# Optimization experiments

Hardware: AMD Instinct MI355X
Metric: run time of the kernel (lower is better)

## Reference

```python
import jax, jax.numpy as jnp
import numpy as np

B, N, E = 16, 1024, 256
H, D = 16, 16            # head_num * qkv_dim == embedding_dim
FF = 2 * E               # ff_size = embedding_dim * 2
EPS = 1e-5


def setup_inputs() -> dict:
    key = jax.random.key(0)
    ks = jax.random.split(key, 12)
    s = lambda fan_in: 1.0 / np.sqrt(fan_in)
    return {
        "x":  jax.random.normal(ks[0], (B, N, E), dtype=jnp.float32),
        # attention projections (nn.Linear, bias=False) stored as [in, out]
        "Wq": jax.random.uniform(ks[1], (E, H * D), jnp.float32, -s(E), s(E)),
        "Wk": jax.random.uniform(ks[2], (E, H * D), jnp.float32, -s(E), s(E)),
        "Wv": jax.random.uniform(ks[3], (E, H * D), jnp.float32, -s(E), s(E)),
        "Wo": jax.random.uniform(ks[4], (H * D, E), jnp.float32, -s(H * D), s(H * D)),
        "bo": jax.random.uniform(ks[5], (E,), jnp.float32, -s(H * D), s(H * D)),
        # InstanceNorm1d affine params
        "gamma1": jnp.ones((E,), jnp.float32),
        "beta1":  jnp.zeros((E,), jnp.float32),
        "gamma2": jnp.ones((E,), jnp.float32),
        "beta2":  jnp.zeros((E,), jnp.float32),
        # SwiGLU FFN: Linear(E, 2*FF) -> SwiGLU -> Linear(FF, E)
        "W1": jax.random.uniform(ks[6], (E, 2 * FF), jnp.float32, -s(E), s(E)),
        "b1": jax.random.uniform(ks[7], (2 * FF,), jnp.float32, -s(E), s(E)),
        "W2": jax.random.uniform(ks[8], (FF, E), jnp.float32, -s(FF), s(FF)),
        "b2": jax.random.uniform(ks[9], (E,), jnp.float32, -s(FF), s(FF)),
    }


def _instance_norm(x, gamma, beta):
    # x: [B, N, E]; normalize over N per (batch, channel), biased variance
    mean = jnp.mean(x, axis=1, keepdims=True)
    var = jnp.mean(jnp.square(x - mean), axis=1, keepdims=True)
    return (x - mean) * jax.lax.rsqrt(var + EPS) * gamma + beta


def reference(x, Wq, Wk, Wv, Wo, bo, gamma1, beta1, gamma2, beta2, W1, b1, W2, b2):
    b, n, e = x.shape
    q = (x @ Wq).reshape(b, n, H, D)
    k = (x @ Wk).reshape(b, n, H, D)
    v = (x @ Wv).reshape(b, n, H, D)
    scores = jnp.einsum("bnhd,bmhd->bhnm", q, k) / np.sqrt(D)   # [B,H,N,N]
    weights = jax.nn.softmax(scores, axis=-1)
    attn = jnp.einsum("bhnm,bmhd->bnhd", weights, v).reshape(b, n, H * D)
    mha = attn @ Wo + bo
    h = _instance_norm(mha + x, gamma1, beta1)
    # SwiGLU FFN: chunk -> (x_part, gate); silu(gate) * x_part
    proj = h @ W1 + b1
    x_part, gate = proj[..., :FF], proj[..., FF:]
    ff = (jax.nn.silu(gate) * x_part) @ W2 + b2
    return _instance_norm(h + ff, gamma2, beta2)
```

## Files before the change

### kernel.cpp

```cpp
#include <hip/hip_runtime.h>
#include <stdint.h>

typedef unsigned short u16;
typedef __bf16 bf16x8 __attribute__((ext_vector_type(8)));
typedef float f32x4 __attribute__((ext_vector_type(4)));

__device__ __forceinline__ float bf2f(u16 v){ return __uint_as_float(((unsigned)v)<<16); }
__device__ __forceinline__ u16 f2bf(float f){
  unsigned u = __float_as_uint(f);
  unsigned r = (u + 0x7FFFu + ((u>>16)&1u)) >> 16;
  return (u16)r;
}
__device__ __forceinline__ float fexp2(float x){
#if __has_builtin(__builtin_amdgcn_exp2f)
  return __builtin_amdgcn_exp2f(x);
#else
  return exp2f(x);
#endif
}

__global__ void transpose_all(const float* __restrict__ Wq, const float* __restrict__ Wk,
                              const float* __restrict__ Wv, const float* __restrict__ Wo,
                              const float* __restrict__ W1, const float* __restrict__ W2,
                              u16* __restrict__ wqkvT, u16* __restrict__ woT,
                              u16* __restrict__ w1T, u16* __restrict__ w2T)
{
  __shared__ u16 tile[32][33];
  int bid = blockIdx.x;
  const float* in; u16* out; int K, N, t2; bool glu = false;
  if (bid < 64)       { in = Wq; out = wqkvT;           K = 256; N = 256;  t2 = bid; }
  else if (bid < 128) { in = Wk; out = wqkvT + 65536;   K = 256; N = 256;  t2 = bid - 64; }
  else if (bid < 192) { in = Wv; out = wqkvT + 131072;  K = 256; N = 256;  t2 = bid - 128; }
  else if (bid < 256) { in = Wo; out = woT;             K = 256; N = 256;  t2 = bid - 192; }
  else if (bid < 512) { in = W1; out = w1T;             K = 256; N = 1024; t2 = bid - 256; glu = true; }
  else                { in = W2; out = w2T;             K = 512; N = 256;  t2 = bid - 512; }
  int ntn = N >> 5;
  int k0 = (t2 / ntn) * 32, n0 = (t2 % ntn) * 32;
  int t = threadIdx.x;
  #pragma unroll
  for (int p = 0; p < 4; ++p) {
    int u = t + p * 256; int r = u >> 5, c = u & 31;
    tile[r][c] = f2bf(in[(size_t)(k0 + r) * N + n0 + c]);
  }
  __syncthreads();
  #pragma unroll
  for (int p = 0; p < 4; ++p) {
    int u = t + p * 256; int r = u >> 5, c = u & 31;
    int q = n0 + r;
    int row = glu ? (q < 512 ? 2 * q : 2 * (q - 512) + 1) : q;
    out[(size_t)row * K + k0 + c] = tile[c][r];
  }
}

__global__ void xconv(const float* __restrict__ x, u16* __restrict__ xb)
{
  int idx = (blockIdx.x * 256 + threadIdx.x) * 8;
  float4 a0 = *(const float4*)(x + idx);
  float4 a1 = *(const float4*)(x + idx + 4);
  union { u16 u[8]; uint4 v; } pk;
  pk.u[0] = f2bf(a0.x); pk.u[1] = f2bf(a0.y); pk.u[2] = f2bf(a0.z); pk.u[3] = f2bf(a0.w);
  pk.u[4] = f2bf(a1.x); pk.u[5] = f2bf(a1.y); pk.u[6] = f2bf(a1.z); pk.u[7] = f2bf(a1.w);
  *(uint4*)(xb + idx) = pk.v;
}

enum { MODE_QKV = 0, MODE_Y_RES = 1, MODE_GLU = 2 };

template<int MODE, int RESF32, int STATS>
__launch_bounds__(256, 2)
__global__ void gemm_kernel(const u16* __restrict__ A, const u16* __restrict__ BT,
                            int M, int N, int K,
                            const float* __restrict__ bias, const void* __restrict__ resp,
                            u16* __restrict__ outB,
                            float* __restrict__ ssum, float* __restrict__ ssq)
{
  __shared__ u16 As[128 * 40];
  __shared__ u16 Bs[128 * 40];
  const int t = threadIdx.x;
  const int m0 = blockIdx.x * 128;
  const int n0 = blockIdx.y * 128;
  const int lane = t & 63;
  const int w = t >> 6;
  const int wm = (w >> 1) * 64;
  const int wn = (w & 1) * 64;
  const int fr = lane & 15;
  const int fg = lane >> 4;

  f32x4 acc[4][4];
  #pragma unroll
  for (int i = 0; i < 4; ++i)
    #pragma unroll
    for (int j = 0; j < 4; ++j)
      acc[i][j] = (f32x4){0.f, 0.f, 0.f, 0.f};

  for (int k0 = 0; k0 < K; k0 += 32) {
    __syncthreads();
    #pragma unroll
    for (int p = 0; p < 2; ++p) {
      int u = t + p * 256;
      int row = u >> 2, cb = u & 3;
      float4 va = *(const float4*)(A + (size_t)(m0 + row) * K + k0 + cb * 8);
      *(float4*)(As + row * 40 + cb * 8) = va;
      float4 vb = *(const float4*)(BT + (size_t)(n0 + row) * K + k0 + cb * 8);
      *(float4*)(Bs + row * 40 + cb * 8) = vb;
    }
    __syncthreads();
    bf16x8 af[4], bfr[4];
    #pragma unroll
    for (int i = 0; i < 4; ++i) af[i]  = *(const bf16x8*)(As + (wm + i * 16 + fr) * 40 + fg * 8);
    #pragma unroll
    for (int j = 0; j < 4; ++j) bfr[j] = *(const bf16x8*)(Bs + (wn + j * 16 + fr) * 40 + fg * 8);
    #pragma unroll
    for (int i = 0; i < 4; ++i)
      #pragma unroll
      for (int j = 0; j < 4; ++j)
        acc[i][j] = __builtin_amdgcn_mfma_f32_16x16x32_bf16(af[i], bfr[j], acc[i][j], 0, 0, 0);
  }

  const int bIdx = m0 >> 10;
  #pragma unroll
  for (int j = 0; j < 4; ++j) {
    int col = n0 + wn + j * 16 + fr;
    float bv = 0.f;
    if (MODE == MODE_Y_RES) bv = bias[col];
    if (MODE == MODE_GLU)   bv = bias[(col >> 1) + ((col & 1) << 9)];
    float sj = 0.f, qj = 0.f;
    #pragma unroll
    for (int i = 0; i < 4; ++i) {
      #pragma unroll
      for (int r = 0; r < 4; ++r) {
        int row = m0 + wm + i * 16 + fg * 4 + r;
        float v = acc[i][j][r] + bv;
        if (MODE == MODE_QKV) {
          int which = col >> 8, h = (col >> 4) & 15, d = col & 15;
          int b = row >> 10, ns = row & 1023;
          outB[(size_t)which * 4194304 + (((size_t)(b * 16 + h) * 1024 + ns) * 16 + d)] = f2bf(v);
        } else if (MODE == MODE_Y_RES) {
          size_t idx = (size_t)row * N + col;
          float rv = RESF32 ? ((const float*)resp)[idx] : bf2f(((const u16*)resp)[idx]);
          float y = v + rv;
          outB[idx] = f2bf(y);
          if (STATS) { sj += y; qj += y * y; }
        } else {
          float partner = __shfl_xor(v, 1);
          if ((fr & 1) == 0) {
            float g = partner / (1.f + __expf(-partner));
            outB[(size_t)row * 512 + (col >> 1)] = f2bf(g * v);
          }
        }
      }
    }
    if (STATS) {
      sj += __shfl_xor(sj, 16); sj += __shfl_xor(sj, 32);
      qj += __shfl_xor(qj, 16); qj += __shfl_xor(qj, 32);
      if (fg == 0) {
        atomicAdd(&ssum[bIdx * 256 + col], sj);
        atomicAdd(&ssq[bIdx * 256 + col], qj);
      }
    }
  }
}

#define SCALE_L2 0.360673760222241f

__launch_bounds__(512, 4)
__global__ void attn_kernel(const u16* __restrict__ Q, const u16* __restrict__ Kg,
                            const u16* __restrict__ Vg, u16* __restrict__ attn)
{
  __shared__ u16 Ks[64 * 24];
  __shared__ u16 Vt[16 * 72];
  __shared__ u16 Pb[8 * 16 * 72];
  const int t = threadIdx.x;
  const int bh = blockIdx.x >> 3;
  const int qg = blockIdx.x & 7;
  const int b = bh >> 4, h = bh & 15;
  const size_t base = (size_t)bh * 16384;
  const int w = t >> 6, lane = t & 63;
  const int fr = lane & 15, fg = lane >> 4;
  u16* Pw = Pb + w * (16 * 72);
  const int q0 = qg * 128 + w * 16;
  const f32x4 zero4 = (f32x4){0.f, 0.f, 0.f, 0.f};

  bf16x8 qf = {};
  if (fg < 2) {
    union { u16 u[8]; uint4 v; bf16x8 f; } qt;
    qt.v = *(const uint4*)(Q + base + (size_t)(q0 + fr) * 16 + fg * 8);
    #pragma unroll
    for (int j = 0; j < 8; ++j) qt.u[j] = f2bf(bf2f(qt.u[j]) * SCALE_L2);
    qf = qt.f;
  }

  f32x4 acco = zero4;
  float lsum[4] = {0.f, 0.f, 0.f, 0.f};

  for (int kc = 0; kc < 1024; kc += 64) {
    __syncthreads();
    if (t < 128) {
      int row = t >> 1, half = t & 1;
      uint4 v = *(const uint4*)(Kg + base + (size_t)(kc + row) * 16 + half * 8);
      *(uint4*)(Ks + row * 24 + half * 8) = v;
    } else if (t < 256) {
      int u = t - 128;
      int row = u >> 1, half = u & 1;
      const u16* src = Vg + base + (size_t)(kc + row) * 16 + half * 8;
      int idx = row & 31, sub = row >> 5;
      int pos = sub * 32 + (idx < 16 ? 2 * idx : 2 * (idx - 16) + 1);
      #pragma unroll
      for (int j = 0; j < 8; ++j) Vt[(half * 8 + j) * 72 + pos] = src[j];
    }
    __syncthreads();

    #pragma unroll
    for (int sub = 0; sub < 2; ++sub) {
      const int kb = sub * 32;
      bf16x8 kf0 = {}, kf1 = {};
      if (fg < 2) {
        kf0 = *(const bf16x8*)(Ks + (kb + fr) * 24 + fg * 8);
        kf1 = *(const bf16x8*)(Ks + (kb + 16 + fr) * 24 + fg * 8);
      }
      f32x4 s0 = __builtin_amdgcn_mfma_f32_16x16x32_bf16(qf, kf0, zero4, 0, 0, 0);
      f32x4 s1 = __builtin_amdgcn_mfma_f32_16x16x32_bf16(qf, kf1, zero4, 0, 0, 0);
      #pragma unroll
      for (int r = 0; r < 4; ++r) {
        float p0 = fexp2(s0[r]);
        float p1 = fexp2(s1[r]);
        lsum[r] += p0 + p1;
        *(unsigned*)(Pw + (fg * 4 + r) * 72 + kb + 2 * fr) =
            __builtin_amdgcn_perm(__float_as_uint(p1), __float_as_uint(p0), 0x07060302u);
      }
      __asm__ volatile("s_waitcnt lgkmcnt(0)" ::: "memory");
      bf16x8 pf = *(const bf16x8*)(Pw + fr * 72 + kb + fg * 8);
      bf16x8 vf = *(const bf16x8*)(Vt + fr * 72 + kb + fg * 8);
      __asm__ volatile("" ::: "memory");
      acco = __builtin_amdgcn_mfma_f32_16x16x32_bf16(pf, vf, acco, 0, 0, 0);
    }
  }

  #pragma unroll
  for (int r = 0; r < 4; ++r) {
    float l = lsum[r];
    l += __shfl_xor(l, 1); l += __shfl_xor(l, 2);
    l += __shfl_xor(l, 4); l += __shfl_xor(l, 8);
    int row = q0 + fg * 4 + r;
    attn[((size_t)(b * 1024 + row)) * 256 + h * 16 + fr] = f2bf(acco[r] / l);
  }
}

template<int OUTBF16>
__global__ void apply_kernel(const u16* __restrict__ y, const float* __restrict__ ssum,
                             const float* __restrict__ ssq, const float* __restrict__ gamma,
                             const float* __restrict__ beta, void* __restrict__ outp)
{
  int idx = (blockIdx.x * 256 + threadIdx.x) * 4;
  int e = idx & 255;
  int b = idx >> 18;
  union { u16 u[4]; uint2 v; } in;
  in.v = *(const uint2*)(y + idx);
  float ov[4];
  const float inv = 1.f / 1024.f;
  #pragma unroll
  for (int j = 0; j < 4; ++j) {
    int ej = e + j;
    float mean = ssum[b * 256 + ej] * inv;
    float var = ssq[b * 256 + ej] * inv - mean * mean;
    float rstd = rsqrtf(var + 1e-5f);
    ov[j] = (bf2f(in.u[j]) - mean) * rstd * gamma[ej] + beta[ej];
  }
  if (OUTBF16) {
    union { u16 u[4]; uint2 v; } pk;
    #pragma unroll
    for (int j = 0; j < 4; ++j) pk.u[j] = f2bf(ov[j]);
    *(uint2*)((u16*)outp + idx) = pk.v;
  } else {
    *(float4*)((float*)outp + idx) = make_float4(ov[0], ov[1], ov[2], ov[3]);
  }
}

extern "C" void kernel_launch(void* const* d_in, const int* in_sizes, int n_in,
                              void* d_out, int out_size, void* d_ws, size_t ws_size,
                              hipStream_t stream)
{
  const float* x      = (const float*)d_in[0];
  const float* Wq     = (const float*)d_in[1];
  const float* Wk     = (const float*)d_in[2];
  const float* Wv     = (const float*)d_in[3];
  const float* Wo     = (const float*)d_in[4];
  const float* bo     = (const float*)d_in[5];
  const float* gamma1 = (const float*)d_in[6];
  const float* beta1  = (const float*)d_in[7];
  const float* gamma2 = (const float*)d_in[8];
  const float* beta2  = (const float*)d_in[9];
  const float* W1     = (const float*)d_in[10];
  const float* b1     = (const float*)d_in[11];
  const float* W2     = (const float*)d_in[12];
  const float* b2     = (const float*)d_in[13];

  char* ws = (char*)d_ws;
  u16*   WQKVT = (u16*)(ws + 0);
  u16*   WOT   = (u16*)(ws + 393216);
  u16*   W1T   = (u16*)(ws + 524288);
  u16*   W2T   = (u16*)(ws + 1048576);
  float* SS    = (float*)(ws + 1310720);
  float* SSUM1 = SS;
  float* SSQ1  = SS + 4096;
  float* SSUM2 = SS + 8192;
  float* SSQ2  = SS + 12288;
  u16*   xb    = (u16*)(ws + 1376256);
  u16*   Qb    = (u16*)(ws + 9764864);
  u16*   ATTN  = (u16*)(ws + 1376256);
  u16*   Y1    = (u16*)(ws + 9764864);
  u16*   Hf    = (u16*)(ws + 26542080);
  u16*   G     = (u16*)(ws + 34930688);
  u16*   Y2    = (u16*)(ws + 1376256);

  hipMemsetAsync(SS, 0, 65536, stream);
  transpose_all<<<640, 256, 0, stream>>>(Wq, Wk, Wv, Wo, W1, W2, WQKVT, WOT, W1T, W2T);
  xconv<<<2048, 256, 0, stream>>>(x, xb);

  gemm_kernel<MODE_QKV, 0, 0><<<dim3(128, 6), 256, 0, stream>>>(
      xb, WQKVT, 16384, 768, 256, nullptr, nullptr, Qb, nullptr, nullptr);

  attn_kernel<<<2048, 512, 0, stream>>>(Qb, Qb + 4194304, Qb + 8388608, ATTN);

  gemm_kernel<MODE_Y_RES, 1, 1><<<dim3(128, 2), 256, 0, stream>>>(
      ATTN, WOT, 16384, 256, 256, bo, x, Y1, SSUM1, SSQ1);

  apply_kernel<1><<<4096, 256, 0, stream>>>(Y1, SSUM1, SSQ1, gamma1, beta1, Hf);

  gemm_kernel<MODE_GLU, 0, 0><<<dim3(128, 8), 256, 0, stream>>>(
      Hf, W1T, 16384, 1024, 256, b1, nullptr, G, nullptr, nullptr);

  gemm_kernel<MODE_Y_RES, 0, 1><<<dim3(128, 2), 256, 0, stream>>>(
      G, W2T, 16384, 256, 512, b2, Hf, Y2, SSUM2, SSQ2);

  apply_kernel<0><<<4096, 256, 0, stream>>>(Y2, SSUM2, SSQ2, gamma2, beta2, (float*)d_out);
}
```

Before: 245.2 us.

## Double-buffer K/V tiles in attention and merge prep kernels

The attention kernel now loads 128-key chunks into double-buffered shared memory, prefetching the next chunk into registers while computing the current one. This halves the number of barriers and hides global load latency. The K rows are permuted instead of V columns so P stays packed per 32-key sub-block, and block order now places heads of the same query group together. Separately, the weight transpose and x conversion kernels are merged into one launch to save launch overhead.

```diff
diff --git a/kernel.cpp b/kernel.cpp
--- a/kernel.cpp
+++ b/kernel.cpp
@@ -19,14 +19,26 @@
 #endif
 }
 
-__global__ void transpose_all(const float* __restrict__ Wq, const float* __restrict__ Wk,
-                              const float* __restrict__ Wv, const float* __restrict__ Wo,
-                              const float* __restrict__ W1, const float* __restrict__ W2,
-                              u16* __restrict__ wqkvT, u16* __restrict__ woT,
-                              u16* __restrict__ w1T, u16* __restrict__ w2T)
-{
+__global__ void prep_kernel(const float* __restrict__ x_, u16* __restrict__ xb,
+                            const float* __restrict__ Wq, const float* __restrict__ Wk,
+                            const float* __restrict__ Wv, const float* __restrict__ Wo,
+                            const float* __restrict__ W1, const float* __restrict__ W2,
+                            u16* __restrict__ wqkvT, u16* __restrict__ woT,
+                            u16* __restrict__ w1T, u16* __restrict__ w2T)
+{
+  int bid = blockIdx.x;
+  int t = threadIdx.x;
+  if (bid >= 640) {
+    int idx = ((bid - 640) * 256 + t) * 8;
+    float4 a0 = *(const float4*)(x_ + idx);
+    float4 a1 = *(const float4*)(x_ + idx + 4);
+    union { u16 u[8]; uint4 v; } pk;
+    pk.u[0] = f2bf(a0.x); pk.u[1] = f2bf(a0.y); pk.u[2] = f2bf(a0.z); pk.u[3] = f2bf(a0.w);
+    pk.u[4] = f2bf(a1.x); pk.u[5] = f2bf(a1.y); pk.u[6] = f2bf(a1.z); pk.u[7] = f2bf(a1.w);
+    *(uint4*)(xb + idx) = pk.v;
+    return;
+  }
   __shared__ u16 tile[32][33];
-  int bid = blockIdx.x;
   const float* in; u16* out; int K, N, t2; bool glu = false;
   if (bid < 64)       { in = Wq; out = wqkvT;           K = 256; N = 256;  t2 = bid; }
   else if (bid < 128) { in = Wk; out = wqkvT + 65536;   K = 256; N = 256;  t2 = bid - 64; }
@@ -36,7 +48,6 @@
   else                { in = W2; out = w2T;             K = 512; N = 256;  t2 = bid - 512; }
   int ntn = N >> 5;
   int k0 = (t2 / ntn) * 32, n0 = (t2 % ntn) * 32;
-  int t = threadIdx.x;
   #pragma unroll
   for (int p = 0; p < 4; ++p) {
     int u = t + p * 256; int r = u >> 5, c = u & 31;
@@ -50,17 +61,6 @@
     int row = glu ? (q < 512 ? 2 * q : 2 * (q - 512) + 1) : q;
     out[(size_t)row * K + k0 + c] = tile[c][r];
   }
-}
-
-__global__ void xconv(const float* __restrict__ x, u16* __restrict__ xb)
-{
-  int idx = (blockIdx.x * 256 + threadIdx.x) * 8;
-  float4 a0 = *(const float4*)(x + idx);
-  float4 a1 = *(const float4*)(x + idx + 4);
-  union { u16 u[8]; uint4 v; } pk;
-  pk.u[0] = f2bf(a0.x); pk.u[1] = f2bf(a0.y); pk.u[2] = f2bf(a0.z); pk.u[3] = f2bf(a0.w);
-  pk.u[4] = f2bf(a1.x); pk.u[5] = f2bf(a1.y); pk.u[6] = f2bf(a1.z); pk.u[7] = f2bf(a1.w);
-  *(uint4*)(xb + idx) = pk.v;
 }
 
 enum { MODE_QKV = 0, MODE_Y_RES = 1, MODE_GLU = 2 };
@@ -166,19 +166,25 @@
 __global__ void attn_kernel(const u16* __restrict__ Q, const u16* __restrict__ Kg,
                             const u16* __restrict__ Vg, u16* __restrict__ attn)
 {
-  __shared__ u16 Ks[64 * 24];
-  __shared__ u16 Vt[16 * 72];
-  __shared__ u16 Pb[8 * 16 * 72];
+  __shared__ u16 Ks[2][128 * 24];
+  __shared__ u16 Vt[2][16 * 136];
+  __shared__ u16 Pb[8][16 * 40];
   const int t = threadIdx.x;
-  const int bh = blockIdx.x >> 3;
-  const int qg = blockIdx.x & 7;
+  const int bh = blockIdx.x & 255;
+  const int qg = blockIdx.x >> 8;
   const int b = bh >> 4, h = bh & 15;
   const size_t base = (size_t)bh * 16384;
   const int w = t >> 6, lane = t & 63;
   const int fr = lane & 15, fg = lane >> 4;
-  u16* Pw = Pb + w * (16 * 72);
+  u16* Pw = Pb[w];
   const int q0 = qg * 128 + w * 16;
   const f32x4 zero4 = (f32x4){0.f, 0.f, 0.f, 0.f};
+
+  const int su = (t & 255) >> 1;
+  const int sh = t & 1;
+  const bool isK = t < 256;
+  const int blk = su >> 5, ii = su & 31;
+  const int kpos = blk * 32 + ((ii & 1) ? 16 + (ii >> 1) : (ii >> 1));
 
   bf16x8 qf = {};
   if (fg < 2) {
@@ -189,33 +195,37 @@
     qf = qt.f;
   }
 
+  {
+    uint4 pre = isK ? *(const uint4*)(Kg + base + (size_t)su * 16 + sh * 8)
+                    : *(const uint4*)(Vg + base + (size_t)su * 16 + sh * 8);
+    if (isK) {
+      *(uint4*)(&Ks[0][kpos * 24 + sh * 8]) = pre;
+    } else {
+      union { u16 u[8]; uint4 v; } pk; pk.v = pre;
+      #pragma unroll
+      for (int j = 0; j < 8; ++j) Vt[0][(sh * 8 + j) * 136 + su] = pk.u[j];
+    }
+  }
+  __syncthreads();
+
   f32x4 acco = zero4;
   float lsum[4] = {0.f, 0.f, 0.f, 0.f};
 
-  for (int kc = 0; kc < 1024; kc += 64) {
-    __syncthreads();
-    if (t < 128) {
-      int row = t >> 1, half = t & 1;
-      uint4 v = *(const uint4*)(Kg + base + (size_t)(kc + row) * 16 + half * 8);
-      *(uint4*)(Ks + row * 24 + half * 8) = v;
-    } else if (t < 256) {
-      int u = t - 128;
-      int row = u >> 1, half = u & 1;
-      const u16* src = Vg + base + (size_t)(kc + row) * 16 + half * 8;
-      int idx = row & 31, sub = row >> 5;
-      int pos = sub * 32 + (idx < 16 ? 2 * idx : 2 * (idx - 16) + 1);
-      #pragma unroll
-      for (int j = 0; j < 8; ++j) Vt[(half * 8 + j) * 72 + pos] = src[j];
-    }
-    __syncthreads();
-
-    #pragma unroll
-    for (int sub = 0; sub < 2; ++sub) {
+  for (int c = 0; c < 8; ++c) {
+    uint4 nxt;
+    if (c < 7) {
+      const size_t off = base + (size_t)((c + 1) * 128 + su) * 16 + sh * 8;
+      nxt = isK ? *(const uint4*)(Kg + off) : *(const uint4*)(Vg + off);
+    }
+    const u16* KsC = Ks[c & 1];
+    const u16* VtC = Vt[c & 1];
+    #pragma unroll
+    for (int sub = 0; sub < 4; ++sub) {
       const int kb = sub * 32;
       bf16x8 kf0 = {}, kf1 = {};
       if (fg < 2) {
-        kf0 = *(const bf16x8*)(Ks + (kb + fr) * 24 + fg * 8);
-        kf1 = *(const bf16x8*)(Ks + (kb + 16 + fr) * 24 + fg * 8);
+        kf0 = *(const bf16x8*)(KsC + (kb + fr) * 24 + fg * 8);
+        kf1 = *(const bf16x8*)(KsC + (kb + 16 + fr) * 24 + fg * 8);
       }
       f32x4 s0 = __builtin_amdgcn_mfma_f32_16x16x32_bf16(qf, kf0, zero4, 0, 0, 0);
       f32x4 s1 = __builtin_amdgcn_mfma_f32_16x16x32_bf16(qf, kf1, zero4, 0, 0, 0);
@@ -224,15 +234,25 @@
         float p0 = fexp2(s0[r]);
         float p1 = fexp2(s1[r]);
         lsum[r] += p0 + p1;
-        *(unsigned*)(Pw + (fg * 4 + r) * 72 + kb + 2 * fr) =
+        *(unsigned*)(Pw + (fg * 4 + r) * 40 + 2 * fr) =
             __builtin_amdgcn_perm(__float_as_uint(p1), __float_as_uint(p0), 0x07060302u);
       }
       __asm__ volatile("s_waitcnt lgkmcnt(0)" ::: "memory");
-      bf16x8 pf = *(const bf16x8*)(Pw + fr * 72 + kb + fg * 8);
-      bf16x8 vf = *(const bf16x8*)(Vt + fr * 72 + kb + fg * 8);
+      bf16x8 pf = *(const bf16x8*)(Pw + fr * 40 + fg * 8);
+      bf16x8 vf = *(const bf16x8*)(VtC + fr * 136 + kb + fg * 8);
       __asm__ volatile("" ::: "memory");
       acco = __builtin_amdgcn_mfma_f32_16x16x32_bf16(pf, vf, acco, 0, 0, 0);
     }
+    if (c < 7) {
+      if (isK) {
+        *(uint4*)(&Ks[(c + 1) & 1][kpos * 24 + sh * 8]) = nxt;
+      } else {
+        union { u16 u[8]; uint4 v; } pk; pk.v = nxt;
+        #pragma unroll
+        for (int j = 0; j < 8; ++j) Vt[(c + 1) & 1][(sh * 8 + j) * 136 + su] = pk.u[j];
+      }
+    }
+    __syncthreads();
   }
 
   #pragma unroll
@@ -313,8 +333,8 @@
   u16*   Y2    = (u16*)(ws + 1376256);
 
   hipMemsetAsync(SS, 0, 65536, stream);
-  transpose_all<<<640, 256, 0, stream>>>(Wq, Wk, Wv, Wo, W1, W2, WQKVT, WOT, W1T, W2T);
-  xconv<<<2048, 256, 0, stream>>>(x, xb);
+  prep_kernel<<<2688, 256, 0, stream>>>(x, xb, Wq, Wk, Wv, Wo, W1, W2,
+                                        WQKVT, WOT, W1T, W2T);
 
   gemm_kernel<MODE_QKV, 0, 0><<<dim3(128, 6), 256, 0, stream>>>(
       xb, WQKVT, 16384, 768, 256, nullptr, nullptr, Qb, nullptr, nullptr);
```

After: 237.7 us. 3.1% less time.
